# Optimization experiments

Hardware: AMD Instinct MI355X
Metric: run time of the kernel (lower is better)

Reference implementation:

```python
import jax, jax.numpy as jnp
import numpy as np

N = 1_000_000
MU_PRIOR = 0.6447


def setup_inputs() -> dict:
    key = jax.random.key(0)
    ks = jax.random.split(key, 8)
    pred_ = jax.random.normal(ks[0], (N, 9), jnp.float32)
    Y_obs = jax.random.normal(ks[1], (N, 9), jnp.float32)
    rrs = jax.random.normal(ks[2], (N, 5), jnp.float32)
    rrs_pred = jax.random.normal(ks[3], (N, 5), jnp.float32)
    nan_array = jax.random.normal(ks[4], (N, 9), jnp.float32)  # all finite -> lens = 9
    # cov_z must be SPD so log(det(cov_z)) is finite
    A = jax.random.normal(ks[5], (N, 3, 3), jnp.float32) * 0.3
    cov_z = jnp.einsum('nij,nkj->nik', A, A) + 0.5 * jnp.eye(3, dtype=jnp.float32)
    mu_z = jax.random.normal(ks[6], (N, 3), jnp.float32)
    parameters = 1.0 + 0.01 * jax.random.normal(ks[7], (64,), jnp.float32)
    return {"pred_": pred_, "Y_obs": Y_obs, "rrs": rrs, "rrs_pred": rrs_pred,
            "nan_array": nan_array, "cov_z": cov_z, "mu_z": mu_z,
            "parameters": parameters}


def reference(pred_, Y_obs, rrs, rrs_pred, nan_array, cov_z, mu_z, parameters):
    n = pred_.shape[0]
    # --- buffers built in __init__ (default multipliers = ones) ---
    se_diag = jnp.asarray([0.0015, 0.0012, 0.001, 0.00086, 0.00057], jnp.float32) ** 2
    rrs_cov_inv = jnp.linalg.inv(jnp.diag(se_diag))            # [5,5]
    Y_cov_inv = jnp.eye(9, dtype=jnp.float32)                  # [9,9]
    s_a = jnp.eye(3, dtype=jnp.float32) * 4.9                  # [3,3]
    s_a_inv = jnp.linalg.inv(s_a)                              # [3,3]

    # trace((X) @ Cinv @ X.T) == sum_n x_n^T Cinv x_n  (trace trick, O(N))
    dr = rrs - rrs_pred                                        # [N,5]
    rrs_error = jnp.einsum('ni,ij,nj->', dr, rrs_cov_inv, dr) / (5.0 * n)

    lens = jnp.sum(~jnp.isnan(nan_array), axis=1).astype(jnp.float32)  # [N]
    dy = pred_ - Y_obs                                         # [N,9]
    obs_quad = jnp.einsum('ni,ij,nj->n', dy, Y_cov_inv, dy)    # [N]
    obs_error = jnp.sum(obs_quad / lens) / n

    # KL(N(mu_z, cov_z) || N(0.6447, s_a)) style term
    logdet_sa = jnp.log(jnp.linalg.det(s_a))
    logdet_cz = jnp.log(jnp.linalg.det(cov_z))                 # [N]
    tr_term = jnp.einsum('ij,nji->n', s_a_inv, cov_z)          # trace(s_a_inv @ cov_z)
    dm = mu_z - MU_PRIOR                                       # [N,3]
    DK = 0.5 * jnp.sum(logdet_sa - logdet_cz + tr_term) / n \
         + 0.5 * jnp.einsum('ni,ij,nj->', dm, s_a_inv, dm) / (3.0 * n)

    l2_norm = jnp.mean((parameters - 1.0) ** 2)
    return rrs_error + 10.0 * obs_error + DK + l2_norm
```

## Files before the change

### kernel.cpp

```cpp
#include <hip/hip_runtime.h>
#include <math.h>

#define MU_PRIOR   0.6447f
#define LOGDET_SA  4.767705615349743f
#define INV_SA     (1.0f/4.9f)

__device__ __forceinline__ float warp_reduce_f(float v) {
#pragma unroll
    for (int off = 32; off > 0; off >>= 1) v += __shfl_down(v, off, 64);
    return v;
}

__device__ __forceinline__ double warp_reduce_d(double v) {
#pragma unroll
    for (int off = 32; off > 0; off >>= 1) v += __shfl_down(v, off, 64);
    return v;
}

__global__ __launch_bounds__(256) void loss_main(
    const float* __restrict__ pred, const float* __restrict__ yobs,
    const float* __restrict__ rrs,  const float* __restrict__ rrsp,
    const float* __restrict__ nanarr, const float* __restrict__ cov,
    const float* __restrict__ mu, double* __restrict__ partial, int rows4)
{
    const int t = blockIdx.x * 256 + threadIdx.x;
    float acc = 0.0f;

    if (t < rows4) {
        const float4* P  = reinterpret_cast<const float4*>(pred)   + (size_t)9 * t;
        const float4* Y  = reinterpret_cast<const float4*>(yobs)   + (size_t)9 * t;
        const float4* NA = reinterpret_cast<const float4*>(nanarr) + (size_t)9 * t;
        const float4* R  = reinterpret_cast<const float4*>(rrs)    + (size_t)5 * t;
        const float4* RP = reinterpret_cast<const float4*>(rrsp)   + (size_t)5 * t;
        const float4* C  = reinterpret_cast<const float4*>(cov)    + (size_t)9 * t;
        const float4* M  = reinterpret_cast<const float4*>(mu)     + (size_t)3 * t;

        float dy2[4]  = {0.f, 0.f, 0.f, 0.f};
        float lens[4] = {0.f, 0.f, 0.f, 0.f};
#pragma unroll
        for (int j = 0; j < 9; ++j) {
            float4 pv = P[j], yv = Y[j], nv = NA[j];
            const float pe[4] = {pv.x, pv.y, pv.z, pv.w};
            const float ye[4] = {yv.x, yv.y, yv.z, yv.w};
            const float ne[4] = {nv.x, nv.y, nv.z, nv.w};
#pragma unroll
            for (int k = 0; k < 4; ++k) {
                const int e = 4 * j + k;
                const int row = e / 9;
                const float d = pe[k] - ye[k];
                dy2[row]  += d * d;
                lens[row] += (ne[k] == ne[k]) ? 1.0f : 0.0f;
            }
        }
        acc += 10.0f * (dy2[0] / lens[0] + dy2[1] / lens[1] +
                        dy2[2] / lens[2] + dy2[3] / lens[3]);

        const float W[5] = {1.0f / (0.0015f * 0.0015f),
                            1.0f / (0.0012f * 0.0012f),
                            1.0f / (0.0010f * 0.0010f),
                            1.0f / (0.00086f * 0.00086f),
                            1.0f / (0.00057f * 0.00057f)};
        float racc = 0.f;
#pragma unroll
        for (int j = 0; j < 5; ++j) {
            float4 rv = R[j], qv = RP[j];
            const float re[4] = {rv.x, rv.y, rv.z, rv.w};
            const float qe[4] = {qv.x, qv.y, qv.z, qv.w};
#pragma unroll
            for (int k = 0; k < 4; ++k) {
                const int e = 4 * j + k;
                const int col = e % 5;
                const float d = re[k] - qe[k];
                racc += d * d * W[col];
            }
        }
        acc += racc * 0.2f;

        float c[36];
#pragma unroll
        for (int j = 0; j < 9; ++j) {
            float4 v = C[j];
            c[4*j] = v.x; c[4*j+1] = v.y; c[4*j+2] = v.z; c[4*j+3] = v.w;
        }
#pragma unroll
        for (int r = 0; r < 4; ++r) {
            const float* m = c + 9 * r;
            const float tr  = m[0] + m[4] + m[8];
            const float det = m[0] * (m[4]*m[8] - m[5]*m[7])
                            - m[1] * (m[3]*m[8] - m[5]*m[6])
                            + m[2] * (m[3]*m[7] - m[4]*m[6]);
            acc += 0.5f * (LOGDET_SA - __logf(det) + tr * INV_SA);
        }

        float dmacc = 0.f;
#pragma unroll
        for (int j = 0; j < 3; ++j) {
            float4 v = M[j];
            const float me[4] = {v.x, v.y, v.z, v.w};
#pragma unroll
            for (int k = 0; k < 4; ++k) {
                const float d = me[k] - MU_PRIOR;
                dmacc += d * d;
            }
        }
        acc += dmacc * (1.0f / 29.4f);
    }

    acc = warp_reduce_f(acc);
    __shared__ float smem[4];
    const int lane = threadIdx.x & 63;
    const int wid  = threadIdx.x >> 6;
    if (lane == 0) smem[wid] = acc;
    __syncthreads();
    if (threadIdx.x == 0)
        partial[blockIdx.x] = (double)(smem[0] + smem[1] + smem[2] + smem[3]);
}

__global__ __launch_bounds__(256) void loss_final(
    const double* __restrict__ partial, int nblocks,
    const float* __restrict__ params, int nparams,
    const float* __restrict__ pred, const float* __restrict__ yobs,
    const float* __restrict__ rrs,  const float* __restrict__ rrsp,
    const float* __restrict__ nanarr, const float* __restrict__ cov,
    const float* __restrict__ mu, int rows, float* __restrict__ out)
{
    const int rows4 = rows >> 2;
    double accA = 0.0;
    double accB = 0.0;

    for (int i = threadIdx.x; i < nblocks; i += 256) accA += partial[i];
    for (int i = threadIdx.x; i < nparams; i += 256) {
        const float d = params[i] - 1.0f;
        accB += (double)(d * d);
    }

    const int r = rows4 * 4 + (int)threadIdx.x;
    if (r < rows) {
        float dy2 = 0.f, len = 0.f;
        for (int i = 0; i < 9; ++i) {
            const float d = pred[9*r + i] - yobs[9*r + i];
            dy2 += d * d;
            const float v = nanarr[9*r + i];
            len += (v == v) ? 1.f : 0.f;
        }
        const float W[5] = {1.0f / (0.0015f * 0.0015f),
                            1.0f / (0.0012f * 0.0012f),
                            1.0f / (0.0010f * 0.0010f),
                            1.0f / (0.00086f * 0.00086f),
                            1.0f / (0.00057f * 0.00057f)};
        float racc = 0.f;
        for (int i = 0; i < 5; ++i) {
            const float d = rrs[5*r + i] - rrsp[5*r + i];
            racc += d * d * W[i];
        }
        const float* m = cov + 9 * (size_t)r;
        const float tr  = m[0] + m[4] + m[8];
        const float det = m[0] * (m[4]*m[8] - m[5]*m[7])
                        - m[1] * (m[3]*m[8] - m[5]*m[6])
                        + m[2] * (m[3]*m[7] - m[4]*m[6]);
        float dm = 0.f;
        for (int i = 0; i < 3; ++i) {
            const float d = mu[3*r + i] - MU_PRIOR;
            dm += d * d;
        }
        accA += (double)(racc * 0.2f + 10.f * dy2 / len
                         + 0.5f * (LOGDET_SA - __logf(det) + tr * INV_SA)
                         + dm * (1.f / 29.4f));
    }

    double val = accA * (1.0 / (double)rows) + accB * (1.0 / (double)nparams);
    val = warp_reduce_d(val);
    __shared__ double sm[4];
    const int lane = threadIdx.x & 63;
    const int wid  = threadIdx.x >> 6;
    if (lane == 0) sm[wid] = val;
    __syncthreads();
    if (threadIdx.x == 0)
        out[0] = (float)(sm[0] + sm[1] + sm[2] + sm[3]);
}

extern "C" void kernel_launch(void* const* d_in, const int* in_sizes, int n_in,
                              void* d_out, int out_size, void* d_ws, size_t ws_size,
                              hipStream_t stream) {
    const float* pred   = (const float*)d_in[0];
    const float* yobs   = (const float*)d_in[1];
    const float* rrs    = (const float*)d_in[2];
    const float* rrsp   = (const float*)d_in[3];
    const float* nanarr = (const float*)d_in[4];
    const float* cov    = (const float*)d_in[5];
    const float* mu     = (const float*)d_in[6];
    const float* params = (const float*)d_in[7];
    float* out = (float*)d_out;

    const int rows  = in_sizes[0] / 9;
    const int rows4 = rows / 4;
    int nblocks = (rows4 + 255) / 256;
    if (nblocks < 1) nblocks = 1;

    double* partial = (double*)d_ws;

    loss_main<<<nblocks, 256, 0, stream>>>(pred, yobs, rrs, rrsp, nanarr, cov, mu,
                                           partial, rows4);
    loss_final<<<1, 256, 0, stream>>>(partial, nblocks, params, in_sizes[7],
                                      pred, yobs, rrs, rrsp, nanarr, cov, mu,
                                      rows, out);
}
```

Before: 222.0 us.

## Stage row blocks through LDS with coalesced float4 loads, one row per thread

Each block now handles 256 rows. The 9-wide arrays (pred, Y_obs, nan mask, cov) are loaded with fully coalesced float4 reads into shared memory, and each thread then computes one row from LDS. The 5-wide and 3-wide terms are reduced straight from coalesced float4 loads using a rotating weight pattern. This removes the strided per-thread 144-byte loads of the old four-rows-per-thread layout, at the cost of 36 KB of LDS per block, which may limit occupancy. Leftover rows are moved into a looped tail in the final kernel.

```diff
diff --git a/kernel.cpp b/kernel.cpp
--- a/kernel.cpp
+++ b/kernel.cpp
@@ -4,6 +4,17 @@
 #define MU_PRIOR   0.6447f
 #define LOGDET_SA  4.767705615349743f
 #define INV_SA     (1.0f/4.9f)
+
+#define CHUNK  256
+#define NF4_9  576
+#define NF4_5  320
+#define NF4_3  192
+
+#define W0 (1.0f / (0.0015f  * 0.0015f))
+#define W1 (1.0f / (0.0012f  * 0.0012f))
+#define W2 (1.0f / (0.0010f  * 0.0010f))
+#define W3 (1.0f / (0.00086f * 0.00086f))
+#define W4 (1.0f / (0.00057f * 0.00057f))
 
 __device__ __forceinline__ float warp_reduce_f(float v) {
 #pragma unroll
@@ -21,98 +32,107 @@
     const float* __restrict__ pred, const float* __restrict__ yobs,
     const float* __restrict__ rrs,  const float* __restrict__ rrsp,
     const float* __restrict__ nanarr, const float* __restrict__ cov,
-    const float* __restrict__ mu, double* __restrict__ partial, int rows4)
+    const float* __restrict__ mu, double* __restrict__ partial)
 {
-    const int t = blockIdx.x * 256 + threadIdx.x;
+    __shared__ float4 sP[NF4_9], sY[NF4_9], sN[NF4_9], sC[NF4_9];
+
+    const int tid = threadIdx.x;
+    const size_t rowBase = (size_t)blockIdx.x * CHUNK;
+
+    const float4* gP = reinterpret_cast<const float4*>(pred   + rowBase * 9);
+    const float4* gY = reinterpret_cast<const float4*>(yobs   + rowBase * 9);
+    const float4* gN = reinterpret_cast<const float4*>(nanarr + rowBase * 9);
+    const float4* gC = reinterpret_cast<const float4*>(cov    + rowBase * 9);
+    const float4* gR = reinterpret_cast<const float4*>(rrs    + rowBase * 5);
+    const float4* gQ = reinterpret_cast<const float4*>(rrsp   + rowBase * 5);
+    const float4* gM = reinterpret_cast<const float4*>(mu     + rowBase * 3);
+
+    {
+        const float4 p0 = gP[tid], p1 = gP[tid + 256];
+        const float4 y0 = gY[tid], y1 = gY[tid + 256];
+        const float4 n0 = gN[tid], n1 = gN[tid + 256];
+        const float4 c0 = gC[tid], c1 = gC[tid + 256];
+        sP[tid] = p0; sP[tid + 256] = p1;
+        sY[tid] = y0; sY[tid + 256] = y1;
+        sN[tid] = n0; sN[tid + 256] = n1;
+        sC[tid] = c0; sC[tid + 256] = c1;
+        if (tid < NF4_9 - 512) {
+            sP[tid + 512] = gP[tid + 512];
+            sY[tid + 512] = gY[tid + 512];
+            sN[tid + 512] = gN[tid + 512];
+            sC[tid + 512] = gC[tid + 512];
+        }
+    }
+
     float acc = 0.0f;
 
-    if (t < rows4) {
-        const float4* P  = reinterpret_cast<const float4*>(pred)   + (size_t)9 * t;
-        const float4* Y  = reinterpret_cast<const float4*>(yobs)   + (size_t)9 * t;
-        const float4* NA = reinterpret_cast<const float4*>(nanarr) + (size_t)9 * t;
-        const float4* R  = reinterpret_cast<const float4*>(rrs)    + (size_t)5 * t;
-        const float4* RP = reinterpret_cast<const float4*>(rrsp)   + (size_t)5 * t;
-        const float4* C  = reinterpret_cast<const float4*>(cov)    + (size_t)9 * t;
-        const float4* M  = reinterpret_cast<const float4*>(mu)     + (size_t)3 * t;
-
-        float dy2[4]  = {0.f, 0.f, 0.f, 0.f};
-        float lens[4] = {0.f, 0.f, 0.f, 0.f};
-#pragma unroll
-        for (int j = 0; j < 9; ++j) {
-            float4 pv = P[j], yv = Y[j], nv = NA[j];
-            const float pe[4] = {pv.x, pv.y, pv.z, pv.w};
-            const float ye[4] = {yv.x, yv.y, yv.z, yv.w};
-            const float ne[4] = {nv.x, nv.y, nv.z, nv.w};
-#pragma unroll
-            for (int k = 0; k < 4; ++k) {
-                const int e = 4 * j + k;
-                const int row = e / 9;
-                const float d = pe[k] - ye[k];
-                dy2[row]  += d * d;
-                lens[row] += (ne[k] == ne[k]) ? 1.0f : 0.0f;
+    {
+        const int w0 = (5 - (tid % 5)) % 5;
+        float ew[5];
+#pragma unroll
+        for (int k = 0; k < 5; ++k) {
+            int idx = w0 + k; if (idx >= 5) idx -= 5;
+            ew[k] = (idx == 0) ? W0 : (idx == 1) ? W1 : (idx == 2) ? W2
+                   : (idx == 3) ? W3 : W4;
+        }
+        float racc = 0.f;
+#pragma unroll
+        for (int j = 0; j < 2; ++j) {
+            const int i = tid + 256 * j;
+            if (j == 0 || i < NF4_5) {
+                const float4 r = gR[i];
+                const float4 q = gQ[i];
+                const int k0 = (5 - j) % 5;
+                const float d0 = r.x - q.x, d1 = r.y - q.y;
+                const float d2 = r.z - q.z, d3 = r.w - q.w;
+                racc += d0 * d0 * ew[(k0    ) % 5];
+                racc += d1 * d1 * ew[(k0 + 1) % 5];
+                racc += d2 * d2 * ew[(k0 + 2) % 5];
+                racc += d3 * d3 * ew[(k0 + 3) % 5];
             }
         }
-        acc += 10.0f * (dy2[0] / lens[0] + dy2[1] / lens[1] +
-                        dy2[2] / lens[2] + dy2[3] / lens[3]);
-
-        const float W[5] = {1.0f / (0.0015f * 0.0015f),
-                            1.0f / (0.0012f * 0.0012f),
-                            1.0f / (0.0010f * 0.0010f),
-                            1.0f / (0.00086f * 0.00086f),
-                            1.0f / (0.00057f * 0.00057f)};
-        float racc = 0.f;
-#pragma unroll
-        for (int j = 0; j < 5; ++j) {
-            float4 rv = R[j], qv = RP[j];
-            const float re[4] = {rv.x, rv.y, rv.z, rv.w};
-            const float qe[4] = {qv.x, qv.y, qv.z, qv.w};
-#pragma unroll
-            for (int k = 0; k < 4; ++k) {
-                const int e = 4 * j + k;
-                const int col = e % 5;
-                const float d = re[k] - qe[k];
-                racc += d * d * W[col];
-            }
-        }
         acc += racc * 0.2f;
-
-        float c[36];
-#pragma unroll
-        for (int j = 0; j < 9; ++j) {
-            float4 v = C[j];
-            c[4*j] = v.x; c[4*j+1] = v.y; c[4*j+2] = v.z; c[4*j+3] = v.w;
-        }
-#pragma unroll
-        for (int r = 0; r < 4; ++r) {
-            const float* m = c + 9 * r;
-            const float tr  = m[0] + m[4] + m[8];
-            const float det = m[0] * (m[4]*m[8] - m[5]*m[7])
-                            - m[1] * (m[3]*m[8] - m[5]*m[6])
-                            + m[2] * (m[3]*m[7] - m[4]*m[6]);
-            acc += 0.5f * (LOGDET_SA - __logf(det) + tr * INV_SA);
-        }
-
-        float dmacc = 0.f;
-#pragma unroll
-        for (int j = 0; j < 3; ++j) {
-            float4 v = M[j];
-            const float me[4] = {v.x, v.y, v.z, v.w};
-#pragma unroll
-            for (int k = 0; k < 4; ++k) {
-                const float d = me[k] - MU_PRIOR;
-                dmacc += d * d;
-            }
-        }
-        acc += dmacc * (1.0f / 29.4f);
+    }
+
+    if (tid < NF4_3) {
+        const float4 v = gM[tid];
+        const float d0 = v.x - MU_PRIOR, d1 = v.y - MU_PRIOR;
+        const float d2 = v.z - MU_PRIOR, d3 = v.w - MU_PRIOR;
+        acc += (d0 * d0 + d1 * d1 + d2 * d2 + d3 * d3) * (1.0f / 29.4f);
+    }
+
+    __syncthreads();
+
+    {
+        const float* p = reinterpret_cast<const float*>(sP) + 9 * tid;
+        const float* y = reinterpret_cast<const float*>(sY) + 9 * tid;
+        const float* a = reinterpret_cast<const float*>(sN) + 9 * tid;
+        const float* m = reinterpret_cast<const float*>(sC) + 9 * tid;
+
+        float dy2 = 0.f, len = 0.f;
+#pragma unroll
+        for (int k = 0; k < 9; ++k) {
+            const float d = p[k] - y[k];
+            dy2 += d * d;
+            const float v = a[k];
+            len += (v == v) ? 1.0f : 0.0f;
+        }
+        acc += 10.0f * dy2 / len;
+
+        const float tr  = m[0] + m[4] + m[8];
+        const float det = m[0] * (m[4] * m[8] - m[5] * m[7])
+                        - m[1] * (m[3] * m[8] - m[5] * m[6])
+                        + m[2] * (m[3] * m[7] - m[4] * m[6]);
+        acc += 0.5f * (LOGDET_SA - __logf(det) + tr * INV_SA);
     }
 
     acc = warp_reduce_f(acc);
     __shared__ float smem[4];
-    const int lane = threadIdx.x & 63;
-    const int wid  = threadIdx.x >> 6;
+    const int lane = tid & 63;
+    const int wid  = tid >> 6;
     if (lane == 0) smem[wid] = acc;
     __syncthreads();
-    if (threadIdx.x == 0)
+    if (tid == 0)
         partial[blockIdx.x] = (double)(smem[0] + smem[1] + smem[2] + smem[3]);
 }
 
@@ -124,7 +144,7 @@
     const float* __restrict__ nanarr, const float* __restrict__ cov,
     const float* __restrict__ mu, int rows, float* __restrict__ out)
 {
-    const int rows4 = rows >> 2;
+    const int mainRows = nblocks * CHUNK;
     double accA = 0.0;
     double accB = 0.0;
 
@@ -134,33 +154,28 @@
         accB += (double)(d * d);
     }
 
-    const int r = rows4 * 4 + (int)threadIdx.x;
-    if (r < rows) {
+    for (int r = mainRows + (int)threadIdx.x; r < rows; r += 256) {
         float dy2 = 0.f, len = 0.f;
         for (int i = 0; i < 9; ++i) {
-            const float d = pred[9*r + i] - yobs[9*r + i];
+            const float d = pred[9 * (size_t)r + i] - yobs[9 * (size_t)r + i];
             dy2 += d * d;
-            const float v = nanarr[9*r + i];
+            const float v = nanarr[9 * (size_t)r + i];
             len += (v == v) ? 1.f : 0.f;
         }
-        const float W[5] = {1.0f / (0.0015f * 0.0015f),
-                            1.0f / (0.0012f * 0.0012f),
-                            1.0f / (0.0010f * 0.0010f),
-                            1.0f / (0.00086f * 0.00086f),
-                            1.0f / (0.00057f * 0.00057f)};
+        const float W[5] = {W0, W1, W2, W3, W4};
         float racc = 0.f;
         for (int i = 0; i < 5; ++i) {
-            const float d = rrs[5*r + i] - rrsp[5*r + i];
+            const float d = rrs[5 * (size_t)r + i] - rrsp[5 * (size_t)r + i];
             racc += d * d * W[i];
         }
         const float* m = cov + 9 * (size_t)r;
         const float tr  = m[0] + m[4] + m[8];
-        const float det = m[0] * (m[4]*m[8] - m[5]*m[7])
-                        - m[1] * (m[3]*m[8] - m[5]*m[6])
-                        + m[2] * (m[3]*m[7] - m[4]*m[6]);
+        const float det = m[0] * (m[4] * m[8] - m[5] * m[7])
+                        - m[1] * (m[3] * m[8] - m[5] * m[6])
+                        + m[2] * (m[3] * m[7] - m[4] * m[6]);
         float dm = 0.f;
         for (int i = 0; i < 3; ++i) {
-            const float d = mu[3*r + i] - MU_PRIOR;
+            const float d = mu[3 * (size_t)r + i] - MU_PRIOR;
             dm += d * d;
         }
         accA += (double)(racc * 0.2f + 10.f * dy2 / len
@@ -192,15 +207,14 @@
     const float* params = (const float*)d_in[7];
     float* out = (float*)d_out;
 
-    const int rows  = in_sizes[0] / 9;
-    const int rows4 = rows / 4;
-    int nblocks = (rows4 + 255) / 256;
-    if (nblocks < 1) nblocks = 1;
+    const int rows    = in_sizes[0] / 9;
+    const int nblocks = rows / CHUNK;
 
     double* partial = (double*)d_ws;
 
-    loss_main<<<nblocks, 256, 0, stream>>>(pred, yobs, rrs, rrsp, nanarr, cov, mu,
-                                           partial, rows4);
+    if (nblocks > 0)
+        loss_main<<<nblocks, 256, 0, stream>>>(pred, yobs, rrs, rrsp, nanarr,
+                                               cov, mu, partial);
     loss_final<<<1, 256, 0, stream>>>(partial, nblocks, params, in_sizes[7],
                                       pred, yobs, rrs, rrsp, nanarr, cov, mu,
                                       rows, out);
```

Result: faster. 209.5 us (-5.6%).
